# Optimization experiments

Hardware: AMD Instinct MI355X
Metric: run time of the kernel (lower is better)

Reference implementation:

```python
import jax, jax.numpy as jnp
from jax import lax
import numpy as np

NSTART, NOPEN, NHID, NCLOSE, NLAYERS, KSZ, N = 40, 128, 256, 3, 40, 9, 1024
H_STEP = 0.1
PAD = (KSZ - 1) // 2  # 4 -> same-length conv
EPS = 1e-5


def conv1(x, K):
    # x: (1, Cin, N), K: (Cout, Cin, k); cross-correlation like torch F.conv1d
    return lax.conv_general_dilated(x, K, (1,), [(PAD, PAD)],
                                    dimension_numbers=('NCH', 'OIH', 'NCH'))


def conv1T(x, K):
    # torch F.conv_transpose1d(x, K, padding=PAD) == conv1d with swapped-channel,
    # flipped kernel and padding k-1-PAD (= PAD here since k=9, PAD=4)
    Kt = jnp.flip(jnp.swapaxes(K, 0, 1), -1)
    return lax.conv_general_dilated(x, Kt, (1,), [(PAD, PAD)],
                                    dimension_numbers=('NCH', 'OIH', 'NCH'))


def instance_norm(x):
    # x: (1, C, N); normalize per channel over spatial dim, biased var, no affine
    m = jnp.mean(x, axis=-1, keepdims=True)
    v = jnp.var(x, axis=-1, keepdims=True)
    return (x - m) * lax.rsqrt(v + EPS)


def get_graph_lap(Z):
    # Z: (C, N). Normalized Gaussian-affinity graph Laplacian.
    sq = jnp.sum(Z * Z, axis=0)  # (N,)
    D2 = jnp.maximum(sq[:, None] + sq[None, :] - 2.0 * (Z.T @ Z), 0.0)
    sigma = jnp.mean(D2) + 1e-12
    Wg = jnp.exp(-D2 / sigma)
    deg = jnp.sum(Wg, axis=1)
    Dh = lax.rsqrt(deg)
    L = Dh[:, None] * (jnp.diag(deg) - Wg) * Dh[None, :]
    return L, deg


def double_sym_layer(Z, Wi, Bi, L):
    # Z: (nopen, N), Wi: (2, nhid, nopen, 9), Bi: (2, nopen, 1), L: (N, N)
    A0 = instance_norm(conv1((Z + Bi[0])[None], Wi[0]))
    A1 = instance_norm((conv1((Z + Bi[1])[None], Wi[1])[0] @ L)[None])
    A0 = jax.nn.relu(A0)
    A1 = jax.nn.relu(A1)
    A0 = conv1T(A0, Wi[0])[0]
    A1 = conv1T(A1, Wi[1])[0] @ L.T
    return A0 + A1  # (nopen, N)


def setup_inputs() -> dict:
    key = jax.random.key(0)
    k1, k2, k3, k4, k5 = jax.random.split(key, 5)
    Z = jax.random.normal(k1, (NSTART, N), dtype=jnp.float32)
    stdv_o = 0.001 * NOPEN / NSTART
    Kopen = jax.random.uniform(k2, (NOPEN, NSTART), minval=-stdv_o, maxval=stdv_o, dtype=jnp.float32)
    stdv_c = 0.001 * NCLOSE / NOPEN
    Kclose = jax.random.uniform(k3, (NCLOSE, NOPEN), minval=-stdv_c, maxval=stdv_c, dtype=jnp.float32)
    W = jax.random.uniform(k4, (NLAYERS, 2, NHID, NOPEN, KSZ), minval=-1e-4, maxval=1e-4, dtype=jnp.float32)
    Bias = jax.random.uniform(k5, (NLAYERS, 2, NOPEN, 1), dtype=jnp.float32) * 1e-4
    return {"Z": Z, "Kopen": Kopen, "Kclose": Kclose, "W": W, "Bias": Bias}


def reference(Z, Kopen, Kclose, W, Bias):
    h = H_STEP
    Zc = Kopen @ Z          # (nopen, N)
    Zold = Zc
    L, _ = get_graph_lap(Zc)
    for i in range(NLAYERS):
        if i % 10 == 0:
            L, _ = get_graph_lap(Zc)
        Ai = double_sym_layer(Zc, W[i], Bias[i], L)
        Zc, Zold = 2.0 * Zc - Zold - (h * h) * Ai, Zc  # leapfrog step
    return (Kclose @ Zc, Kclose @ Zold)
```

## Files before the change

kernel.cpp:

```cpp
#include <hip/hip_runtime.h>

#define NN 1024
#define NOPEN 128
#define NHID 256
#define NSTART 40
#define NCLOSE 3
#define NLAYERS 40
#define KSZ 9

static constexpr float H2 = 0.01f;
static constexpr float IN_EPS = 1e-5f;

using floatx4 = __attribute__((ext_vector_type(4))) float;
using bfrag = __attribute__((ext_vector_type(8))) short;

__device__ __forceinline__ ushort f2bf(float f) {
    union { float f; unsigned u; } v; v.f = f;
    unsigned r = v.u + 0x7fffu + ((v.u >> 16) & 1u);
    return (ushort)(r >> 16);
}

__device__ __forceinline__ void prepw_piece(const float* __restrict__ W, ushort* __restrict__ Wt,
                                            ushort* __restrict__ WtT, int lb, int lsrc, int tid) {
    if (lb < 72) {
        int q = lb; int coq = q & 3; q >>= 2; int t = q % 9, z = q / 9;
        const float* Wz = W + (size_t)(lsrc * 2 + z) * (NHID * NOPEN * KSZ);
        ushort* Wo = Wt + ((size_t)z * 9 + t) * (NHID * NOPEN);
#pragma unroll
        for (int r = 0; r < 32; ++r) {
            int idx = r * 256 + tid;
            int co = coq * 64 + (idx >> 7), ci = idx & 127;
            Wo[co * NOPEN + ci] = f2bf(Wz[co * (NOPEN * KSZ) + ci * KSZ + t]);
        }
    } else {
        int q = lb - 72; int ciq = q & 3; q >>= 2; int t = q % 9, z = q / 9;
        const float* Wz = W + (size_t)(lsrc * 2 + z) * (NHID * NOPEN * KSZ);
        ushort* Wo = WtT + ((size_t)z * 9 + t) * (NOPEN * NHID);
#pragma unroll
        for (int r = 0; r < 32; ++r) {
            int idx = r * 256 + tid;
            int ci = ciq * 32 + (idx >> 8), co = idx & 255;
            Wo[ci * NHID + co] = f2bf(Wz[co * (NOPEN * KSZ) + ci * KSZ + t]);
        }
    }
}

__global__ __launch_bounds__(256) void k_open(const float* __restrict__ Kopen, const float* __restrict__ Z,
                       float* __restrict__ Zc, float* __restrict__ Zold,
                       const float* __restrict__ Bias0, ushort* __restrict__ Zct,
                       ushort* __restrict__ At0, ushort* __restrict__ At1,
                       const float* __restrict__ W, ushort* __restrict__ Wt,
                       ushort* __restrict__ WtT, float* __restrict__ sig) {
    const int v = blockIdx.x, tid = threadIdx.x;
    if (v < 512) {
        int o = v >> 2, n = (v & 3) * 256 + tid;
        float acc = 0.f;
#pragma unroll
        for (int s = 0; s < NSTART; ++s)
            acc = fmaf(Kopen[o * NSTART + s], Z[s * NN + n], acc);
        Zc[o * NN + n] = acc;
        Zold[o * NN + n] = acc;
#pragma unroll
        for (int z = 0; z < 2; ++z)
            Zct[z * (1032 * 128) + (n + 4) * 128 + o] = f2bf(acc + Bias0[z * NOPEN + o]);
    } else if (v < 656) {
        prepw_piece(W, Wt, WtT, v - 512, 0, tid);
    } else {
        if (tid == 0) sig[0] = 0.f;
        for (int idx = tid; idx < 1024; idx += 256) {
            int z = idx >> 9, rr = idx & 511;
            ushort* Zz = Zct + z * (1032 * 128);
            Zz[rr] = 0; Zz[1028 * 128 + rr] = 0;
        }
        for (int idx = tid; idx < 2048; idx += 256) {
            int a = idx >> 10, rr = idx & 1023;
            ushort* A = a ? At1 : At0;
            A[rr] = 0; A[1028 * 256 + rr] = 0;
        }
    }
}

__global__ __launch_bounds__(256) void k_d2(const float* __restrict__ Zc,
                                            float* __restrict__ D2, float* __restrict__ sig) {
    __shared__ __align__(16) float Zi[32 * 36];
    __shared__ __align__(16) float Zj[32 * 68];
    __shared__ float sqi[32], sqj[64];
    __shared__ float red[4];
    const int tid = threadIdx.x;
    const int tx = tid & 15, ty = tid >> 4;
    const int j0 = blockIdx.x * 64, i0 = blockIdx.y * 32;
    if (tid < 32) sqi[tid] = 0.f;
    else if (tid < 96) sqj[tid - 32] = 0.f;
    float acc[2][4] = {};
    for (int c0 = 0; c0 < NOPEN; c0 += 32) {
        for (int idx = tid; idx < 32 * 32; idx += 256) {
            int c = idx >> 5, ii = idx & 31;
            Zi[c * 36 + ii] = Zc[(c0 + c) * NN + i0 + ii];
        }
        for (int idx = tid; idx < 32 * 64; idx += 256) {
            int c = idx >> 6, jj = idx & 63;
            Zj[c * 68 + jj] = Zc[(c0 + c) * NN + j0 + jj];
        }
        __syncthreads();
        if (tid < 32) {
            float s = 0.f;
            for (int c = 0; c < 32; ++c) { float x = Zi[c * 36 + tid]; s = fmaf(x, x, s); }
            sqi[tid] += s;
        } else if (tid < 96) {
            int jj = tid - 32;
            float s = 0.f;
            for (int c = 0; c < 32; ++c) { float x = Zj[c * 68 + jj]; s = fmaf(x, x, s); }
            sqj[jj] += s;
        }
#pragma unroll 8
        for (int c = 0; c < 32; ++c) {
            float2 zi = *(const float2*)&Zi[c * 36 + ty * 2];
            float4 zj = *(const float4*)&Zj[c * 68 + tx * 4];
            acc[0][0] = fmaf(zi.x, zj.x, acc[0][0]);
            acc[0][1] = fmaf(zi.x, zj.y, acc[0][1]);
            acc[0][2] = fmaf(zi.x, zj.z, acc[0][2]);
            acc[0][3] = fmaf(zi.x, zj.w, acc[0][3]);
            acc[1][0] = fmaf(zi.y, zj.x, acc[1][0]);
            acc[1][1] = fmaf(zi.y, zj.y, acc[1][1]);
            acc[1][2] = fmaf(zi.y, zj.z, acc[1][2]);
            acc[1][3] = fmaf(zi.y, zj.w, acc[1][3]);
        }
        __syncthreads();
    }
    float part = 0.f;
#pragma unroll
    for (int m = 0; m < 2; ++m) {
        int i = i0 + ty * 2 + m;
        float sqi_v = sqi[ty * 2 + m];
        float4 d;
        d.x = fmaxf(sqi_v + sqj[tx * 4 + 0] - 2.f * acc[m][0], 0.f);
        d.y = fmaxf(sqi_v + sqj[tx * 4 + 1] - 2.f * acc[m][1], 0.f);
        d.z = fmaxf(sqi_v + sqj[tx * 4 + 2] - 2.f * acc[m][2], 0.f);
        d.w = fmaxf(sqi_v + sqj[tx * 4 + 3] - 2.f * acc[m][3], 0.f);
        *(float4*)&D2[(size_t)i * NN + j0 + tx * 4] = d;
        part += (d.x + d.y) + (d.z + d.w);
    }
#pragma unroll
    for (int off = 32; off > 0; off >>= 1) part += __shfl_down(part, off);
    if ((tid & 63) == 0) red[tid >> 6] = part;
    __syncthreads();
    if (tid == 0) atomicAdd(sig, red[0] + red[1] + red[2] + red[3]);
}

__global__ void k_deg(const float* __restrict__ D2, const float* __restrict__ sig,
                      float* __restrict__ Dh) {
    __shared__ float red[4];
    int i = blockIdx.x, tid = threadIdx.x;
    float inv = 1.f / (sig[0] * (1.f / 1048576.f) + 1e-12f);
    float4 v = *(const float4*)&D2[(size_t)i * NN + tid * 4];
    float s = __expf(-v.x * inv) + __expf(-v.y * inv) + __expf(-v.z * inv) + __expf(-v.w * inv);
#pragma unroll
    for (int off = 32; off > 0; off >>= 1) s += __shfl_down(s, off);
    if ((tid & 63) == 0) red[tid >> 6] = s;
    __syncthreads();
    if (tid == 0) Dh[i] = rsqrtf(red[0] + red[1] + red[2] + red[3]);
}

__global__ void k_L(const float* __restrict__ D2, const float* __restrict__ sig,
                    const float* __restrict__ Dh, ushort* __restrict__ Lb) {
    int i = blockIdx.x, tid = threadIdx.x;
    int j = tid * 4;
    float inv = 1.f / (sig[0] * (1.f / 1048576.f) + 1e-12f);
    float dhi = Dh[i];
    float4 v = *(const float4*)&D2[(size_t)i * NN + j];
    float4 dj = *(const float4*)&Dh[j];
    float4 o;
    o.x = -dhi * dj.x * __expf(-v.x * inv);
    o.y = -dhi * dj.y * __expf(-v.y * inv);
    o.z = -dhi * dj.z * __expf(-v.z * inv);
    o.w = -dhi * dj.w * __expf(-v.w * inv);
    if (i == j + 0) o.x += 1.f;
    if (i == j + 1) o.y += 1.f;
    if (i == j + 2) o.z += 1.f;
    if (i == j + 3) o.w += 1.f;
    ushort4 ob; ob.x = f2bf(o.x); ob.y = f2bf(o.y); ob.z = f2bf(o.z); ob.w = f2bf(o.w);
    *(ushort4*)&Lb[(size_t)i * NN + j] = ob;
}

__global__ __launch_bounds__(256) void k_conv(const ushort* __restrict__ Zct,
        const ushort* __restrict__ Wt, float* __restrict__ C0, ushort* __restrict__ C1b) {
    const int z = blockIdx.z;
    const int p0 = blockIdx.x * 64, co0 = blockIdx.y * 32;
    __shared__ ushort Xs[72 * 136];
    __shared__ ushort Wl[9 * 32 * 136];
    const int tid = threadIdx.x;
    const ushort* Zz = Zct + z * (1032 * 128);
    const ushort* Wz = Wt + (size_t)z * 9 * NHID * NOPEN;
    for (int idx = tid; idx < 1152; idx += 256) {
        int row = idx >> 4, ch = (idx & 15) * 8;
        *(bfrag*)&Xs[row * 136 + ch] = *(const bfrag*)&Zz[(p0 + row) * 128 + ch];
    }
    for (int idx = tid; idx < 4608; idx += 256) {
        int t = idx >> 9, rem = idx & 511;
        int c = rem >> 4, ch = (rem & 15) * 8;
        *(bfrag*)&Wl[(t * 32 + c) * 136 + ch] = *(const bfrag*)&Wz[(t * NHID + co0 + c) * 128 + ch];
    }
    __syncthreads();
    const int l = tid & 63, wv = tid >> 6;
    const int wm = wv >> 1, wn = wv & 1;
    const int lm = l & 15, lq = l >> 4;
    floatx4 acc[2] = {};
    for (int t = 0; t < 9; ++t) {
        const int wbase = (t * 32 + wm * 16 + lm) * 136 + lq * 8;
        const int xbase = (wn * 32 + lm + t) * 136 + lq * 8;
#pragma unroll
        for (int kc = 0; kc < 4; ++kc) {
            bfrag a = *(const bfrag*)&Wl[wbase + kc * 32];
            bfrag b0 = *(const bfrag*)&Xs[xbase + kc * 32];
            acc[0] = __builtin_amdgcn_mfma_f32_16x16x32_bf16(a, b0, acc[0], 0, 0, 0);
            bfrag b1 = *(const bfrag*)&Xs[xbase + 16 * 136 + kc * 32];
            acc[1] = __builtin_amdgcn_mfma_f32_16x16x32_bf16(a, b1, acc[1], 0, 0, 0);
        }
    }
    const int cog = co0 + wm * 16 + lq * 4;
    const int pg = p0 + wn * 32 + lm;
#pragma unroll
    for (int j = 0; j < 2; ++j)
#pragma unroll
        for (int r = 0; r < 4; ++r) {
            if (z == 0) C0[(cog + r) * NN + pg + j * 16] = acc[j][r];
            else        C1b[(cog + r) * NN + pg + j * 16] = f2bf(acc[j][r]);
        }
}

__global__ __launch_bounds__(256) void k_xl_mfma(const ushort* __restrict__ X,
                                                 const ushort* __restrict__ Lb,
                                                 float* __restrict__ P, int M) {
    __shared__ __align__(16) ushort As[64 * 136];
    __shared__ __align__(16) ushort Bs[128 * 136];
    const int tid = threadIdx.x;
    const int lane = tid & 63, wave = tid >> 6;
    const int wm = wave >> 1, wn = wave & 1;
    const int n0 = blockIdx.x * 128, m0 = blockIdx.y * 64, kc = blockIdx.z * 128;
    {
        int q = tid;
#pragma unroll
        for (int r = 0; r < 4; ++r, q += 256) {
            int row = q >> 4, ch = (q & 15) * 8;
            *(bfrag*)&As[row * 136 + ch] = *(const bfrag*)&X[(m0 + row) * NN + kc + ch];
        }
        q = tid;
#pragma unroll
        for (int r = 0; r < 8; ++r, q += 256) {
            int row = q >> 4, ch = (q & 15) * 8;
            *(bfrag*)&Bs[row * 136 + ch] = *(const bfrag*)&Lb[(n0 + row) * NN + kc + ch];
        }
    }
    __syncthreads();
    floatx4 acc[2][4] = {};
    const int lrow = (lane & 15) * 136;
    const int koff = (lane >> 4) * 8;
#pragma unroll
    for (int ks = 0; ks < 4; ++ks) {
        bfrag a[2], b[4];
#pragma unroll
        for (int i = 0; i < 2; ++i)
            a[i] = *(const bfrag*)&As[(wm * 32 + i * 16) * 136 + lrow + ks * 32 + koff];
#pragma unroll
        for (int j = 0; j < 4; ++j)
            b[j] = *(const bfrag*)&Bs[(wn * 64 + j * 16) * 136 + lrow + ks * 32 + koff];
#pragma unroll
        for (int i = 0; i < 2; ++i)
#pragma unroll
            for (int j = 0; j < 4; ++j)
                acc[i][j] = __builtin_amdgcn_mfma_f32_16x16x32_bf16(a[i], b[j], acc[i][j], 0, 0, 0);
    }
    const int mg0 = m0 + wm * 32 + (lane >> 4) * 4;
    const int ng0 = n0 + wn * 64 + (lane & 15);
    const size_t base = (size_t)blockIdx.z * M * NN;
#pragma unroll
    for (int i = 0; i < 2; ++i)
#pragma unroll
        for (int j = 0; j < 4; ++j)
#pragma unroll
            for (int r = 0; r < 4; ++r)
                P[base + (size_t)(mg0 + i * 16 + r) * NN + ng0 + j * 16] = acc[i][j][r];
}

__global__ void k_inorm(const float* __restrict__ C0, const float* __restrict__ P1,
                        float* __restrict__ A1sum, float* __restrict__ Mu, float* __restrict__ Rs) {
    const int c = blockIdx.x, arr = blockIdx.y, tid = threadIdx.x;
    __shared__ float rs[4], rq[4];
    float4 v;
    if (arr == 0) {
        v = *(const float4*)&C0[c * NN + tid * 4];
    } else {
        v.x = v.y = v.z = v.w = 0.f;
#pragma unroll
        for (int s = 0; s < 8; ++s) {
            float4 p = *(const float4*)&P1[(size_t)(s * NHID + c) * NN + tid * 4];
            v.x += p.x; v.y += p.y; v.z += p.z; v.w += p.w;
        }
        *(float4*)&A1sum[c * NN + tid * 4] = v;
    }
    float s = (v.x + v.y) + (v.z + v.w);
    float q = (v.x * v.x + v.y * v.y) + (v.z * v.z + v.w * v.w);
#pragma unroll
    for (int off = 32; off > 0; off >>= 1) { s += __shfl_down(s, off); q += __shfl_down(q, off); }
    if ((tid & 63) == 0) { rs[tid >> 6] = s; rq[tid >> 6] = q; }
    __syncthreads();
    if (tid == 0) {
        float S = rs[0] + rs[1] + rs[2] + rs[3];
        float Q = rq[0] + rq[1] + rq[2] + rq[3];
        float mean = S * (1.f / NN);
        float var = Q * (1.f / NN) - mean * mean;
        Mu[arr * NHID + c] = mean;
        Rs[arr * NHID + c] = rsqrtf(var + IN_EPS);
    }
}

__global__ __launch_bounds__(256) void k_normT(const float* __restrict__ C0,
        const float* __restrict__ A1sum, const float* __restrict__ Mu, const float* __restrict__ Rs,
        ushort* __restrict__ At0, ushort* __restrict__ At1) {
    const int arr = blockIdx.z;
    const int p0 = blockIdx.x * 64, co0 = blockIdx.y * 64;
    const float* in = arr ? A1sum : C0;
    ushort* out = arr ? At1 : At0;
    __shared__ ushort Ls[64 * 72];
    const int tid = threadIdx.x;
#pragma unroll
    for (int r = 0; r < 4; ++r) {
        int idx = r * 256 + tid;
        int col = idx >> 4, pq = idx & 15;
        int co = co0 + col;
        float4 v = *(const float4*)&in[(size_t)co * NN + p0 + pq * 4];
        float m = Mu[arr * NHID + co], sc = Rs[arr * NHID + co];
        Ls[(pq * 4 + 0) * 72 + col] = f2bf(fmaxf((v.x - m) * sc, 0.f));
        Ls[(pq * 4 + 1) * 72 + col] = f2bf(fmaxf((v.y - m) * sc, 0.f));
        Ls[(pq * 4 + 2) * 72 + col] = f2bf(fmaxf((v.z - m) * sc, 0.f));
        Ls[(pq * 4 + 3) * 72 + col] = f2bf(fmaxf((v.w - m) * sc, 0.f));
    }
    __syncthreads();
#pragma unroll
    for (int r = 0; r < 2; ++r) {
        int idx = r * 256 + tid;
        int row = idx >> 3, ch = (idx & 7) * 8;
        *(bfrag*)&out[(size_t)(p0 + row + 4) * 256 + co0 + ch] = *(const bfrag*)&Ls[row * 72 + ch];
    }
}

__global__ __launch_bounds__(256) void k_convT(const ushort* __restrict__ At0,
        const ushort* __restrict__ At1, const ushort* __restrict__ WtT,
        float* __restrict__ Tacc, ushort* __restrict__ T1b) {
    const int z = blockIdx.z;
    const int p0 = blockIdx.x * 64, ci0 = blockIdx.y * 16;
    __shared__ ushort Al[72 * 264];
    __shared__ ushort Wl[9 * 16 * 264];
    const ushort* A = z ? At1 : At0;
    const ushort* Wz = WtT + (size_t)z * 9 * NOPEN * NHID;
    const int tid = threadIdx.x;
    for (int idx = tid; idx < 2304; idx += 256) {
        int row = idx >> 5, ch = (idx & 31) * 8;
        *(bfrag*)&Al[row * 264 + ch] = *(const bfrag*)&A[(p0 + row) * 256 + ch];
    }
    for (int idx = tid; idx < 4608; idx += 256) {
        int t = idx >> 9, rem = idx & 511;
        int c = rem >> 5, ch = (rem & 31) * 8;
        *(bfrag*)&Wl[(t * 16 + c) * 264 + ch] = *(const bfrag*)&Wz[(t * NOPEN + ci0 + c) * 256 + ch];
    }
    __syncthreads();
    const int l = tid & 63, wv = tid >> 6;
    const int lm = l & 15, lq = l >> 4;
    floatx4 acc0 = {}, acc1 = {};
    for (int t = 0; t < 9; ++t) {
        const int abase = (wv * 16 + lm + 8 - t) * 264 + lq * 8;
        const int wbase = (t * 16 + lm) * 264 + lq * 8;
#pragma unroll
        for (int kc = 0; kc < 8; kc += 2) {
            bfrag a0 = *(const bfrag*)&Wl[wbase + kc * 32];
            bfrag b0 = *(const bfrag*)&Al[abase + kc * 32];
            acc0 = __builtin_amdgcn_mfma_f32_16x16x32_bf16(a0, b0, acc0, 0, 0, 0);
            bfrag a1 = *(const bfrag*)&Wl[wbase + kc * 32 + 32];
            bfrag b1 = *(const bfrag*)&Al[abase + kc * 32 + 32];
            acc1 = __builtin_amdgcn_mfma_f32_16x16x32_bf16(a1, b1, acc1, 0, 0, 0);
        }
    }
    floatx4 acc = acc0 + acc1;
    const int cig = ci0 + lq * 4;
    const int pg = p0 + wv * 16 + lm;
#pragma unroll
    for (int r = 0; r < 4; ++r) {
        if (z == 0) Tacc[(cig + r) * NN + pg] = acc[r];
        else        T1b[(cig + r) * NN + pg] = f2bf(acc[r]);
    }
}

__global__ __launch_bounds__(256) void k_leap(const float* __restrict__ P2,
        const float* __restrict__ Tacc, const float* __restrict__ Zc, float* __restrict__ Zo,
        const float* __restrict__ BiasN, ushort* __restrict__ Zct,
        const float* __restrict__ W, ushort* __restrict__ Wt, ushort* __restrict__ WtT,
        float* __restrict__ sig, int lnext, int doprep) {
    const int v = blockIdx.x, tid = threadIdx.x;
    if (v < 128) {
        int off = (v * 256 + tid) * 4;
        float4 a = *(const float4*)&Tacc[off];
#pragma unroll
        for (int s = 0; s < 8; ++s) {
            float4 p = *(const float4*)&P2[(size_t)(s << 17) + off];
            a.x += p.x; a.y += p.y; a.z += p.z; a.w += p.w;
        }
        float4 zc = *(const float4*)&Zc[off];
        float4 zo = *(const float4*)&Zo[off];
        float4 zn;
        zn.x = 2.f * zc.x - zo.x - H2 * a.x;
        zn.y = 2.f * zc.y - zo.y - H2 * a.y;
        zn.z = 2.f * zc.z - zo.z - H2 * a.z;
        zn.w = 2.f * zc.w - zo.w - H2 * a.w;
        *(float4*)&Zo[off] = zn;
        int ci = off >> 10, n = off & 1023;
#pragma unroll
        for (int z = 0; z < 2; ++z) {
            float bz = BiasN[z * NOPEN + ci];
            ushort* Zz = Zct + z * (1032 * 128);
            Zz[(n + 4) * 128 + ci] = f2bf(zn.x + bz);
            Zz[(n + 5) * 128 + ci] = f2bf(zn.y + bz);
            Zz[(n + 6) * 128 + ci] = f2bf(zn.z + bz);
            Zz[(n + 7) * 128 + ci] = f2bf(zn.w + bz);
        }
    } else if (v < 272) {
        if (doprep) prepw_piece(W, Wt, WtT, v - 128, lnext, tid);
    } else {
        if (tid == 0) sig[0] = 0.f;
    }
}

__global__ void k_close(const float* __restrict__ Kclose, const float* __restrict__ Zc,
                        const float* __restrict__ Zold, float* __restrict__ out) {
    int n = blockIdx.x * 256 + threadIdx.x;
    int o = blockIdx.y;
    const float* Zb = blockIdx.z ? Zold : Zc;
    float a = 0.f;
#pragma unroll
    for (int c = 0; c < NOPEN; ++c) a = fmaf(Kclose[o * NOPEN + c], Zb[c * NN + n], a);
    out[blockIdx.z * (NCLOSE * NN) + o * NN + n] = a;
}

extern "C" void kernel_launch(void* const* d_in, const int* in_sizes, int n_in,
                              void* d_out, int out_size, void* d_ws, size_t ws_size,
                              hipStream_t stream) {
    const float* Z      = (const float*)d_in[0];
    const float* Kopen  = (const float*)d_in[1];
    const float* Kclose = (const float*)d_in[2];
    const float* W      = (const float*)d_in[3];
    const float* Bias   = (const float*)d_in[4];
    float* out = (float*)d_out;
    float* ws  = (float*)d_ws;

    float* Zb0   = ws + 0;
    float* Zb1   = ws + 131072;
    float* D2    = ws + 262144;
    float* C0    = ws + 1310720;
    float* A1sum = ws + 1572864;
    float* Tacc  = ws + 1835008;
    float* P1    = ws + 1966080;
    float* P2    = ws + 4063232;
    float* Dh    = ws + 5111808;
    float* sig   = ws + 5112832;
    float* Mu    = ws + 5113856;
    float* Rs    = ws + 5114880;
    ushort* Lb  = (ushort*)(ws + 5115904);
    ushort* C1b = (ushort*)(ws + 5640192);
    ushort* T1b = (ushort*)(ws + 5771264);
    ushort* Zct = (ushort*)(ws + 5836800);
    ushort* At0 = (ushort*)(ws + 5968896);
    ushort* At1 = (ushort*)(ws + 6100992);
    ushort* Wt  = (ushort*)(ws + 6233088);
    ushort* WtT = (ushort*)(ws + 6528000);

    k_open<<<dim3(657), 256, 0, stream>>>(Kopen, Z, Zb0, Zb1, Bias, Zct, At0, At1,
                                          W, Wt, WtT, sig);

    float* Zc = Zb0;
    float* Zold = Zb1;
    for (int i = 0; i < NLAYERS; ++i) {
        if (i % 10 == 0) {
            k_d2<<<dim3(16, 32), 256, 0, stream>>>(Zc, D2, sig);
            k_deg<<<dim3(NN), 256, 0, stream>>>(D2, sig, Dh);
            k_L<<<dim3(NN), 256, 0, stream>>>(D2, sig, Dh, Lb);
        }
        k_conv<<<dim3(16, 8, 2), 256, 0, stream>>>(Zct, Wt, C0, C1b);
        k_xl_mfma<<<dim3(8, 4, 8), 256, 0, stream>>>(C1b, Lb, P1, NHID);
        k_inorm<<<dim3(NHID, 2), 256, 0, stream>>>(C0, P1, A1sum, Mu, Rs);
        k_normT<<<dim3(16, 4, 2), 256, 0, stream>>>(C0, A1sum, Mu, Rs, At0, At1);
        k_convT<<<dim3(16, 8, 2), 256, 0, stream>>>(At0, At1, WtT, Tacc, T1b);
        k_xl_mfma<<<dim3(8, 2, 8), 256, 0, stream>>>(T1b, Lb, P2, NOPEN);
        int lnext = (i + 1 < NLAYERS) ? i + 1 : NLAYERS - 1;
        k_leap<<<dim3(273), 256, 0, stream>>>(P2, Tacc, Zc, Zold,
                                              Bias + (size_t)lnext * 2 * NOPEN, Zct,
                                              W, Wt, WtT, sig, lnext, (i + 1 < NLAYERS) ? 1 : 0);
        float* tmp = Zc; Zc = Zold; Zold = tmp;
    }

    k_close<<<dim3(4, NCLOSE, 2), 256, 0, stream>>>(Kclose, Zc, Zold, out);
}
```

Baseline: 2.122 ms.

## Restructure layer pipeline: fuse leapfrog into conv, merge norm into GEMM kernels, atomic accumulate

Reworks each layer's kernel sequence. The leapfrog update moves into the next layer's conv input staging, using a 3-buffer rotation and a point-major (n,128) layout for Z. Instance-norm and transpose work is merged into the L-GEMM and convT kernels, and the second L-GEMM accumulates into Tacc with atomics instead of writing split-K partials. This cuts the launches per layer from 7 to 5 and removes the P2, A1sum and Zct buffers. In exchange it adds atomic contention, recomputes the leapfrog expression redundantly in every conv block, and changes summation order.

```diff
diff --git a/kernel.cpp b/kernel.cpp
--- a/kernel.cpp
+++ b/kernel.cpp
@@ -46,11 +46,9 @@
 }
 
 __global__ __launch_bounds__(256) void k_open(const float* __restrict__ Kopen, const float* __restrict__ Z,
-                       float* __restrict__ Zc, float* __restrict__ Zold,
-                       const float* __restrict__ Bias0, ushort* __restrict__ Zct,
-                       ushort* __restrict__ At0, ushort* __restrict__ At1,
+                       float* __restrict__ B0, ushort* __restrict__ At0, ushort* __restrict__ At1,
                        const float* __restrict__ W, ushort* __restrict__ Wt,
-                       ushort* __restrict__ WtT, float* __restrict__ sig) {
+                       ushort* __restrict__ WtT, float* __restrict__ Tacc, float* __restrict__ sig) {
     const int v = blockIdx.x, tid = threadIdx.x;
     if (v < 512) {
         int o = v >> 2, n = (v & 3) * 256 + tid;
@@ -58,29 +56,23 @@
 #pragma unroll
         for (int s = 0; s < NSTART; ++s)
             acc = fmaf(Kopen[o * NSTART + s], Z[s * NN + n], acc);
-        Zc[o * NN + n] = acc;
-        Zold[o * NN + n] = acc;
-#pragma unroll
-        for (int z = 0; z < 2; ++z)
-            Zct[z * (1032 * 128) + (n + 4) * 128 + o] = f2bf(acc + Bias0[z * NOPEN + o]);
+        B0[n * 128 + o] = acc;
     } else if (v < 656) {
         prepw_piece(W, Wt, WtT, v - 512, 0, tid);
-    } else {
+    } else if (v == 656) {
         if (tid == 0) sig[0] = 0.f;
-        for (int idx = tid; idx < 1024; idx += 256) {
-            int z = idx >> 9, rr = idx & 511;
-            ushort* Zz = Zct + z * (1032 * 128);
-            Zz[rr] = 0; Zz[1028 * 128 + rr] = 0;
-        }
         for (int idx = tid; idx < 2048; idx += 256) {
             int a = idx >> 10, rr = idx & 1023;
             ushort* A = a ? At1 : At0;
             A[rr] = 0; A[1028 * 256 + rr] = 0;
         }
-    }
-}
-
-__global__ __launch_bounds__(256) void k_d2(const float* __restrict__ Zc,
+    } else {
+        int w = v - 657;
+        *(float4*)&Tacc[(w * 256 + tid) * 4] = float4{0.f, 0.f, 0.f, 0.f};
+    }
+}
+
+__global__ __launch_bounds__(256) void k_d2(const float* __restrict__ Zcur,
                                             float* __restrict__ D2, float* __restrict__ sig) {
     __shared__ __align__(16) float Zi[32 * 36];
     __shared__ __align__(16) float Zj[32 * 68];
@@ -94,12 +86,12 @@
     float acc[2][4] = {};
     for (int c0 = 0; c0 < NOPEN; c0 += 32) {
         for (int idx = tid; idx < 32 * 32; idx += 256) {
-            int c = idx >> 5, ii = idx & 31;
-            Zi[c * 36 + ii] = Zc[(c0 + c) * NN + i0 + ii];
+            int c = idx & 31, ii = idx >> 5;
+            Zi[c * 36 + ii] = Zcur[(i0 + ii) * 128 + c0 + c];
         }
         for (int idx = tid; idx < 32 * 64; idx += 256) {
-            int c = idx >> 6, jj = idx & 63;
-            Zj[c * 68 + jj] = Zc[(c0 + c) * NN + j0 + jj];
+            int c = idx & 31, jj = idx >> 5;
+            Zj[c * 68 + jj] = Zcur[(j0 + jj) * 128 + c0 + c];
         }
         __syncthreads();
         if (tid < 32) {
@@ -182,23 +174,51 @@
     *(ushort4*)&Lb[(size_t)i * NN + j] = ob;
 }
 
-__global__ __launch_bounds__(256) void k_conv(const ushort* __restrict__ Zct,
+__global__ __launch_bounds__(256) void k_conv2(const float* __restrict__ Zc, const float* __restrict__ Zo,
+        const float* __restrict__ Ta, float* __restrict__ Zn, const float* __restrict__ BiasL,
         const ushort* __restrict__ Wt, float* __restrict__ C0, ushort* __restrict__ C1b) {
     const int z = blockIdx.z;
     const int p0 = blockIdx.x * 64, co0 = blockIdx.y * 32;
     __shared__ ushort Xs[72 * 136];
     __shared__ ushort Wl[9 * 32 * 136];
     const int tid = threadIdx.x;
-    const ushort* Zz = Zct + z * (1032 * 128);
+    const float* Bz = BiasL + z * NOPEN;
     const ushort* Wz = Wt + (size_t)z * 9 * NHID * NOPEN;
-    for (int idx = tid; idx < 1152; idx += 256) {
-        int row = idx >> 4, ch = (idx & 15) * 8;
-        *(bfrag*)&Xs[row * 136 + ch] = *(const bfrag*)&Zz[(p0 + row) * 128 + ch];
+    for (int idx = tid; idx < 72 * 32; idx += 256) {
+        int row = idx >> 5, ci = (idx & 31) * 4;
+        int n = p0 - 4 + row;
+        ushort4 o4 = {0, 0, 0, 0};
+        if ((unsigned)n < (unsigned)NN) {
+            float4 zc = *(const float4*)&Zc[n * 128 + ci];
+            float4 zo = *(const float4*)&Zo[n * 128 + ci];
+            float4 ta = *(const float4*)&Ta[n * 128 + ci];
+            float4 bb = *(const float4*)&Bz[ci];
+            o4.x = f2bf(2.f * zc.x - zo.x - H2 * ta.x + bb.x);
+            o4.y = f2bf(2.f * zc.y - zo.y - H2 * ta.y + bb.y);
+            o4.z = f2bf(2.f * zc.z - zo.z - H2 * ta.z + bb.z);
+            o4.w = f2bf(2.f * zc.w - zo.w - H2 * ta.w + bb.w);
+        }
+        *(ushort4*)&Xs[row * 136 + ci] = o4;
     }
     for (int idx = tid; idx < 4608; idx += 256) {
         int t = idx >> 9, rem = idx & 511;
         int c = rem >> 4, ch = (rem & 15) * 8;
         *(bfrag*)&Wl[(t * 32 + c) * 136 + ch] = *(const bfrag*)&Wz[(t * NHID + co0 + c) * 128 + ch];
+    }
+    if (blockIdx.y == 0 && z == 0) {
+        for (int idx = tid; idx < 64 * 32; idx += 256) {
+            int row = idx >> 5, ci = (idx & 31) * 4;
+            int n = p0 + row;
+            float4 zc = *(const float4*)&Zc[n * 128 + ci];
+            float4 zo = *(const float4*)&Zo[n * 128 + ci];
+            float4 ta = *(const float4*)&Ta[n * 128 + ci];
+            float4 o;
+            o.x = 2.f * zc.x - zo.x - H2 * ta.x;
+            o.y = 2.f * zc.y - zo.y - H2 * ta.y;
+            o.z = 2.f * zc.z - zo.z - H2 * ta.z;
+            o.w = 2.f * zc.w - zo.w - H2 * ta.w;
+            *(float4*)&Zn[n * 128 + ci] = o;
+        }
     }
     __syncthreads();
     const int l = tid & 63, wv = tid >> 6;
@@ -228,21 +248,22 @@
         }
 }
 
-__global__ __launch_bounds__(256) void k_xl_mfma(const ushort* __restrict__ X,
-                                                 const ushort* __restrict__ Lb,
-                                                 float* __restrict__ P, int M) {
-    __shared__ __align__(16) ushort As[64 * 136];
-    __shared__ __align__(16) ushort Bs[128 * 136];
-    const int tid = threadIdx.x;
-    const int lane = tid & 63, wave = tid >> 6;
-    const int wm = wave >> 1, wn = wave & 1;
-    const int n0 = blockIdx.x * 128, m0 = blockIdx.y * 64, kc = blockIdx.z * 128;
-    {
+__global__ __launch_bounds__(256) void k_s2(const ushort* __restrict__ C1b,
+        const ushort* __restrict__ Lb, float* __restrict__ P1,
+        const float* __restrict__ C0, ushort* __restrict__ At0) {
+    __shared__ __align__(16) ushort sm[26112];
+    const int bid = blockIdx.x, tid = threadIdx.x;
+    if (bid < 256) {
+        ushort* As = sm;
+        ushort* Bs = sm + 8704;
+        const int lane = tid & 63, wave = tid >> 6;
+        const int wm = wave >> 1, wn = wave & 1;
+        const int n0 = (bid & 7) * 128, m0 = ((bid >> 3) & 3) * 64, kc = (bid >> 5) * 128;
         int q = tid;
 #pragma unroll
         for (int r = 0; r < 4; ++r, q += 256) {
             int row = q >> 4, ch = (q & 15) * 8;
-            *(bfrag*)&As[row * 136 + ch] = *(const bfrag*)&X[(m0 + row) * NN + kc + ch];
+            *(bfrag*)&As[row * 136 + ch] = *(const bfrag*)&C1b[(m0 + row) * NN + kc + ch];
         }
         q = tid;
 #pragma unroll
@@ -250,110 +271,64 @@
             int row = q >> 4, ch = (q & 15) * 8;
             *(bfrag*)&Bs[row * 136 + ch] = *(const bfrag*)&Lb[(n0 + row) * NN + kc + ch];
         }
-    }
-    __syncthreads();
-    floatx4 acc[2][4] = {};
-    const int lrow = (lane & 15) * 136;
-    const int koff = (lane >> 4) * 8;
-#pragma unroll
-    for (int ks = 0; ks < 4; ++ks) {
-        bfrag a[2], b[4];
+        __syncthreads();
+        floatx4 acc[2][4] = {};
+        const int lrow = (lane & 15) * 136;
+        const int koff = (lane >> 4) * 8;
+#pragma unroll
+        for (int ks = 0; ks < 4; ++ks) {
+            bfrag a[2], b[4];
+#pragma unroll
+            for (int i = 0; i < 2; ++i)
+                a[i] = *(const bfrag*)&As[(wm * 32 + i * 16) * 136 + lrow + ks * 32 + koff];
+#pragma unroll
+            for (int j = 0; j < 4; ++j)
+                b[j] = *(const bfrag*)&Bs[(wn * 64 + j * 16) * 136 + lrow + ks * 32 + koff];
+#pragma unroll
+            for (int i = 0; i < 2; ++i)
+#pragma unroll
+                for (int j = 0; j < 4; ++j)
+                    acc[i][j] = __builtin_amdgcn_mfma_f32_16x16x32_bf16(a[i], b[j], acc[i][j], 0, 0, 0);
+        }
+        const int mg0 = m0 + wm * 32 + (lane >> 4) * 4;
+        const int ng0 = n0 + wn * 64 + (lane & 15);
+        const size_t base = (size_t)(bid >> 5) * NHID * NN;
 #pragma unroll
         for (int i = 0; i < 2; ++i)
-            a[i] = *(const bfrag*)&As[(wm * 32 + i * 16) * 136 + lrow + ks * 32 + koff];
-#pragma unroll
-        for (int j = 0; j < 4; ++j)
-            b[j] = *(const bfrag*)&Bs[(wn * 64 + j * 16) * 136 + lrow + ks * 32 + koff];
-#pragma unroll
-        for (int i = 0; i < 2; ++i)
 #pragma unroll
             for (int j = 0; j < 4; ++j)
-                acc[i][j] = __builtin_amdgcn_mfma_f32_16x16x32_bf16(a[i], b[j], acc[i][j], 0, 0, 0);
-    }
-    const int mg0 = m0 + wm * 32 + (lane >> 4) * 4;
-    const int ng0 = n0 + wn * 64 + (lane & 15);
-    const size_t base = (size_t)blockIdx.z * M * NN;
-#pragma unroll
-    for (int i = 0; i < 2; ++i)
-#pragma unroll
-        for (int j = 0; j < 4; ++j)
-#pragma unroll
-            for (int r = 0; r < 4; ++r)
-                P[base + (size_t)(mg0 + i * 16 + r) * NN + ng0 + j * 16] = acc[i][j][r];
-}
-
-__global__ void k_inorm(const float* __restrict__ C0, const float* __restrict__ P1,
-                        float* __restrict__ A1sum, float* __restrict__ Mu, float* __restrict__ Rs) {
-    const int c = blockIdx.x, arr = blockIdx.y, tid = threadIdx.x;
-    __shared__ float rs[4], rq[4];
-    float4 v;
-    if (arr == 0) {
-        v = *(const float4*)&C0[c * NN + tid * 4];
-    } else {
-        v.x = v.y = v.z = v.w = 0.f;
-#pragma unroll
-        for (int s = 0; s < 8; ++s) {
-            float4 p = *(const float4*)&P1[(size_t)(s * NHID + c) * NN + tid * 4];
-            v.x += p.x; v.y += p.y; v.z += p.z; v.w += p.w;
-        }
-        *(float4*)&A1sum[c * NN + tid * 4] = v;
-    }
-    float s = (v.x + v.y) + (v.z + v.w);
-    float q = (v.x * v.x + v.y * v.y) + (v.z * v.z + v.w * v.w);
-#pragma unroll
-    for (int off = 32; off > 0; off >>= 1) { s += __shfl_down(s, off); q += __shfl_down(q, off); }
-    if ((tid & 63) == 0) { rs[tid >> 6] = s; rq[tid >> 6] = q; }
-    __syncthreads();
-    if (tid == 0) {
+#pragma unroll
+                for (int r = 0; r < 4; ++r)
+                    P1[base + (size_t)(mg0 + i * 16 + r) * NN + ng0 + j * 16] = acc[i][j][r];
+    } else {
+        float* rs = (float*)sm;
+        float* rq = rs + 4;
+        const int c = bid - 256;
+        float4 v = *(const float4*)&C0[(size_t)c * NN + tid * 4];
+        float s = (v.x + v.y) + (v.z + v.w);
+        float qq = (v.x * v.x + v.y * v.y) + (v.z * v.z + v.w * v.w);
+#pragma unroll
+        for (int off = 32; off > 0; off >>= 1) { s += __shfl_down(s, off); qq += __shfl_down(qq, off); }
+        if ((tid & 63) == 0) { rs[tid >> 6] = s; rq[tid >> 6] = qq; }
+        __syncthreads();
         float S = rs[0] + rs[1] + rs[2] + rs[3];
         float Q = rq[0] + rq[1] + rq[2] + rq[3];
         float mean = S * (1.f / NN);
-        float var = Q * (1.f / NN) - mean * mean;
-        Mu[arr * NHID + c] = mean;
-        Rs[arr * NHID + c] = rsqrtf(var + IN_EPS);
-    }
-}
-
-__global__ __launch_bounds__(256) void k_normT(const float* __restrict__ C0,
-        const float* __restrict__ A1sum, const float* __restrict__ Mu, const float* __restrict__ Rs,
-        ushort* __restrict__ At0, ushort* __restrict__ At1) {
-    const int arr = blockIdx.z;
-    const int p0 = blockIdx.x * 64, co0 = blockIdx.y * 64;
-    const float* in = arr ? A1sum : C0;
-    ushort* out = arr ? At1 : At0;
-    __shared__ ushort Ls[64 * 72];
-    const int tid = threadIdx.x;
-#pragma unroll
-    for (int r = 0; r < 4; ++r) {
-        int idx = r * 256 + tid;
-        int col = idx >> 4, pq = idx & 15;
-        int co = co0 + col;
-        float4 v = *(const float4*)&in[(size_t)co * NN + p0 + pq * 4];
-        float m = Mu[arr * NHID + co], sc = Rs[arr * NHID + co];
-        Ls[(pq * 4 + 0) * 72 + col] = f2bf(fmaxf((v.x - m) * sc, 0.f));
-        Ls[(pq * 4 + 1) * 72 + col] = f2bf(fmaxf((v.y - m) * sc, 0.f));
-        Ls[(pq * 4 + 2) * 72 + col] = f2bf(fmaxf((v.z - m) * sc, 0.f));
-        Ls[(pq * 4 + 3) * 72 + col] = f2bf(fmaxf((v.w - m) * sc, 0.f));
-    }
-    __syncthreads();
-#pragma unroll
-    for (int r = 0; r < 2; ++r) {
-        int idx = r * 256 + tid;
-        int row = idx >> 3, ch = (idx & 7) * 8;
-        *(bfrag*)&out[(size_t)(p0 + row + 4) * 256 + co0 + ch] = *(const bfrag*)&Ls[row * 72 + ch];
-    }
-}
-
-__global__ __launch_bounds__(256) void k_convT(const ushort* __restrict__ At0,
-        const ushort* __restrict__ At1, const ushort* __restrict__ WtT,
-        float* __restrict__ Tacc, ushort* __restrict__ T1b) {
-    const int z = blockIdx.z;
-    const int p0 = blockIdx.x * 64, ci0 = blockIdx.y * 16;
-    __shared__ ushort Al[72 * 264];
-    __shared__ ushort Wl[9 * 16 * 264];
-    const ushort* A = z ? At1 : At0;
-    const ushort* Wz = WtT + (size_t)z * 9 * NOPEN * NHID;
-    const int tid = threadIdx.x;
+        float rstd = rsqrtf(Q * (1.f / NN) - mean * mean + IN_EPS);
+        int p = tid * 4;
+        At0[(p + 4) * 256 + c] = f2bf(fmaxf((v.x - mean) * rstd, 0.f));
+        At0[(p + 5) * 256 + c] = f2bf(fmaxf((v.y - mean) * rstd, 0.f));
+        At0[(p + 6) * 256 + c] = f2bf(fmaxf((v.z - mean) * rstd, 0.f));
+        At0[(p + 7) * 256 + c] = f2bf(fmaxf((v.w - mean) * rstd, 0.f));
+    }
+}
+
+__device__ __forceinline__ void convT_body(int b, const ushort* __restrict__ A,
+        const ushort* __restrict__ Wz, ushort* sm, int tid, floatx4& acc, int& cig, int& pg) {
+    const int pt = b & 15, cit = b >> 4;
+    const int p0 = pt * 64, ci0 = cit * 16;
+    ushort* Al = sm;
+    ushort* Wl = sm + 19008;
     for (int idx = tid; idx < 2304; idx += 256) {
         int row = idx >> 5, ch = (idx & 31) * 8;
         *(bfrag*)&Al[row * 264 + ch] = *(const bfrag*)&A[(p0 + row) * 256 + ch];
@@ -380,64 +355,150 @@
             acc1 = __builtin_amdgcn_mfma_f32_16x16x32_bf16(a1, b1, acc1, 0, 0, 0);
         }
     }
-    floatx4 acc = acc0 + acc1;
-    const int cig = ci0 + lq * 4;
-    const int pg = p0 + wv * 16 + lm;
-#pragma unroll
-    for (int r = 0; r < 4; ++r) {
-        if (z == 0) Tacc[(cig + r) * NN + pg] = acc[r];
-        else        T1b[(cig + r) * NN + pg] = f2bf(acc[r]);
-    }
-}
-
-__global__ __launch_bounds__(256) void k_leap(const float* __restrict__ P2,
-        const float* __restrict__ Tacc, const float* __restrict__ Zc, float* __restrict__ Zo,
-        const float* __restrict__ BiasN, ushort* __restrict__ Zct,
-        const float* __restrict__ W, ushort* __restrict__ Wt, ushort* __restrict__ WtT,
-        float* __restrict__ sig, int lnext, int doprep) {
-    const int v = blockIdx.x, tid = threadIdx.x;
-    if (v < 128) {
-        int off = (v * 256 + tid) * 4;
-        float4 a = *(const float4*)&Tacc[off];
+    acc = acc0 + acc1;
+    cig = ci0 + lq * 4;
+    pg = p0 + wv * 16 + lm;
+}
+
+__global__ __launch_bounds__(256) void k_s3(const ushort* __restrict__ At0,
+        const ushort* __restrict__ WtT, float* __restrict__ Tacc,
+        const float* __restrict__ P1, ushort* __restrict__ At1) {
+    __shared__ __align__(16) ushort sm[57024];
+    const int bid = blockIdx.x, tid = threadIdx.x;
+    if (bid < 128) {
+        floatx4 acc; int cig, pg;
+        convT_body(bid, At0, WtT, sm, tid, acc, cig, pg);
+#pragma unroll
+        for (int r = 0; r < 4; ++r)
+            Tacc[pg * 128 + cig + r] = acc[r];
+    } else {
+        float* rs = (float*)sm;
+        float* rq = rs + 4;
+        const int c = bid - 128;
+        float4 v = {0.f, 0.f, 0.f, 0.f};
 #pragma unroll
         for (int s = 0; s < 8; ++s) {
-            float4 p = *(const float4*)&P2[(size_t)(s << 17) + off];
-            a.x += p.x; a.y += p.y; a.z += p.z; a.w += p.w;
-        }
-        float4 zc = *(const float4*)&Zc[off];
-        float4 zo = *(const float4*)&Zo[off];
-        float4 zn;
-        zn.x = 2.f * zc.x - zo.x - H2 * a.x;
-        zn.y = 2.f * zc.y - zo.y - H2 * a.y;
-        zn.z = 2.f * zc.z - zo.z - H2 * a.z;
-        zn.w = 2.f * zc.w - zo.w - H2 * a.w;
-        *(float4*)&Zo[off] = zn;
-        int ci = off >> 10, n = off & 1023;
-#pragma unroll
-        for (int z = 0; z < 2; ++z) {
-            float bz = BiasN[z * NOPEN + ci];
-            ushort* Zz = Zct + z * (1032 * 128);
-            Zz[(n + 4) * 128 + ci] = f2bf(zn.x + bz);
-            Zz[(n + 5) * 128 + ci] = f2bf(zn.y + bz);
-            Zz[(n + 6) * 128 + ci] = f2bf(zn.z + bz);
-            Zz[(n + 7) * 128 + ci] = f2bf(zn.w + bz);
-        }
-    } else if (v < 272) {
-        if (doprep) prepw_piece(W, Wt, WtT, v - 128, lnext, tid);
+            float4 p = *(const float4*)&P1[(size_t)(s * NHID + c) * NN + tid * 4];
+            v.x += p.x; v.y += p.y; v.z += p.z; v.w += p.w;
+        }
+        float s = (v.x + v.y) + (v.z + v.w);
+        float qq = (v.x * v.x + v.y * v.y) + (v.z * v.z + v.w * v.w);
+#pragma unroll
+        for (int off = 32; off > 0; off >>= 1) { s += __shfl_down(s, off); qq += __shfl_down(qq, off); }
+        if ((tid & 63) == 0) { rs[tid >> 6] = s; rq[tid >> 6] = qq; }
+        __syncthreads();
+        float S = rs[0] + rs[1] + rs[2] + rs[3];
+        float Q = rq[0] + rq[1] + rq[2] + rq[3];
+        float mean = S * (1.f / NN);
+        float rstd = rsqrtf(Q * (1.f / NN) - mean * mean + IN_EPS);
+        int p = tid * 4;
+        At1[(p + 4) * 256 + c] = f2bf(fmaxf((v.x - mean) * rstd, 0.f));
+        At1[(p + 5) * 256 + c] = f2bf(fmaxf((v.y - mean) * rstd, 0.f));
+        At1[(p + 6) * 256 + c] = f2bf(fmaxf((v.z - mean) * rstd, 0.f));
+        At1[(p + 7) * 256 + c] = f2bf(fmaxf((v.w - mean) * rstd, 0.f));
+    }
+}
+
+__global__ __launch_bounds__(256) void k_s4(const ushort* __restrict__ At1,
+        const ushort* __restrict__ WtT, ushort* __restrict__ T1b,
+        const float* __restrict__ W, ushort* __restrict__ Wt, ushort* __restrict__ WtT_w,
+        int lnext, int doprep) {
+    __shared__ __align__(16) ushort sm[57024];
+    const int bid = blockIdx.x, tid = threadIdx.x;
+    if (bid < 128) {
+        floatx4 acc; int cig, pg;
+        convT_body(bid, At1, WtT + (size_t)9 * NOPEN * NHID, sm, tid, acc, cig, pg);
+#pragma unroll
+        for (int r = 0; r < 4; ++r)
+            T1b[(cig + r) * NN + pg] = f2bf(acc[r]);
+    } else {
+        if (doprep) prepw_piece(W, Wt, WtT_w, bid - 128, lnext, tid);
+    }
+}
+
+__global__ __launch_bounds__(256) void k_s5(const ushort* __restrict__ T1b,
+        const ushort* __restrict__ Lb, float* __restrict__ Tacc, float* __restrict__ sig) {
+    __shared__ __align__(16) ushort sm[26112];
+    const int bid = blockIdx.x, tid = threadIdx.x;
+    if (bid < 128) {
+        ushort* As = sm;
+        ushort* Bs = sm + 8704;
+        const int lane = tid & 63, wave = tid >> 6;
+        const int wm = wave >> 1, wn = wave & 1;
+        const int n0 = (bid & 7) * 128, m0 = ((bid >> 3) & 1) * 64, kc = (bid >> 4) * 128;
+        int q = tid;
+#pragma unroll
+        for (int r = 0; r < 4; ++r, q += 256) {
+            int row = q >> 4, ch = (q & 15) * 8;
+            *(bfrag*)&As[row * 136 + ch] = *(const bfrag*)&T1b[(m0 + row) * NN + kc + ch];
+        }
+        q = tid;
+#pragma unroll
+        for (int r = 0; r < 8; ++r, q += 256) {
+            int row = q >> 4, ch = (q & 15) * 8;
+            *(bfrag*)&Bs[row * 136 + ch] = *(const bfrag*)&Lb[(n0 + row) * NN + kc + ch];
+        }
+        __syncthreads();
+        floatx4 acc[2][4] = {};
+        const int lrow = (lane & 15) * 136;
+        const int koff = (lane >> 4) * 8;
+#pragma unroll
+        for (int ks = 0; ks < 4; ++ks) {
+            bfrag a[2], b[4];
+#pragma unroll
+            for (int i = 0; i < 2; ++i)
+                a[i] = *(const bfrag*)&As[(wm * 32 + i * 16) * 136 + lrow + ks * 32 + koff];
+#pragma unroll
+            for (int j = 0; j < 4; ++j)
+                b[j] = *(const bfrag*)&Bs[(wn * 64 + j * 16) * 136 + lrow + ks * 32 + koff];
+#pragma unroll
+            for (int i = 0; i < 2; ++i)
+#pragma unroll
+                for (int j = 0; j < 4; ++j)
+                    acc[i][j] = __builtin_amdgcn_mfma_f32_16x16x32_bf16(a[i], b[j], acc[i][j], 0, 0, 0);
+        }
+        const int mg0 = m0 + wm * 32 + (lane >> 4) * 4;
+        const int ng0 = n0 + wn * 64 + (lane & 15);
+#pragma unroll
+        for (int i = 0; i < 2; ++i)
+#pragma unroll
+            for (int j = 0; j < 4; ++j)
+#pragma unroll
+                for (int r = 0; r < 4; ++r)
+                    atomicAdd(&Tacc[(ng0 + j * 16) * 128 + mg0 + i * 16 + r], acc[i][j][r]);
     } else {
         if (tid == 0) sig[0] = 0.f;
     }
 }
 
 __global__ void k_close(const float* __restrict__ Kclose, const float* __restrict__ Zc,
-                        const float* __restrict__ Zold, float* __restrict__ out) {
+                        const float* __restrict__ Zo, const float* __restrict__ Ta,
+                        float* __restrict__ out) {
     int n = blockIdx.x * 256 + threadIdx.x;
-    int o = blockIdx.y;
-    const float* Zb = blockIdx.z ? Zold : Zc;
+    int o = blockIdx.y, zsel = blockIdx.z;
     float a = 0.f;
-#pragma unroll
-    for (int c = 0; c < NOPEN; ++c) a = fmaf(Kclose[o * NOPEN + c], Zb[c * NN + n], a);
-    out[blockIdx.z * (NCLOSE * NN) + o * NN + n] = a;
+    if (zsel == 0) {
+#pragma unroll
+        for (int c4 = 0; c4 < 32; ++c4) {
+            float4 zc = *(const float4*)&Zc[n * 128 + c4 * 4];
+            float4 zo = *(const float4*)&Zo[n * 128 + c4 * 4];
+            float4 ta = *(const float4*)&Ta[n * 128 + c4 * 4];
+            float4 k = *(const float4*)&Kclose[o * 128 + c4 * 4];
+            a = fmaf(k.x, 2.f * zc.x - zo.x - H2 * ta.x, a);
+            a = fmaf(k.y, 2.f * zc.y - zo.y - H2 * ta.y, a);
+            a = fmaf(k.z, 2.f * zc.z - zo.z - H2 * ta.z, a);
+            a = fmaf(k.w, 2.f * zc.w - zo.w - H2 * ta.w, a);
+        }
+    } else {
+#pragma unroll
+        for (int c4 = 0; c4 < 32; ++c4) {
+            float4 zc = *(const float4*)&Zc[n * 128 + c4 * 4];
+            float4 k = *(const float4*)&Kclose[o * 128 + c4 * 4];
+            a = fmaf(k.x, zc.x, a); a = fmaf(k.y, zc.y, a);
+            a = fmaf(k.z, zc.z, a); a = fmaf(k.w, zc.w, a);
+        }
+    }
+    out[zsel * (NCLOSE * NN) + o * NN + n] = a;
 }
 
 extern "C" void kernel_launch(void* const* d_in, const int* in_sizes, int n_in,
@@ -451,50 +512,50 @@
     float* out = (float*)d_out;
     float* ws  = (float*)d_ws;
 
-    float* Zb0   = ws + 0;
-    float* Zb1   = ws + 131072;
-    float* D2    = ws + 262144;
-    float* C0    = ws + 1310720;
-    float* A1sum = ws + 1572864;
-    float* Tacc  = ws + 1835008;
-    float* P1    = ws + 1966080;
-    float* P2    = ws + 4063232;
-    float* Dh    = ws + 5111808;
-    float* sig   = ws + 5112832;
-    float* Mu    = ws + 5113856;
-    float* Rs    = ws + 5114880;
-    ushort* Lb  = (ushort*)(ws + 5115904);
-    ushort* C1b = (ushort*)(ws + 5640192);
-    ushort* T1b = (ushort*)(ws + 5771264);
-    ushort* Zct = (ushort*)(ws + 5836800);
-    ushort* At0 = (ushort*)(ws + 5968896);
-    ushort* At1 = (ushort*)(ws + 6100992);
-    ushort* Wt  = (ushort*)(ws + 6233088);
-    ushort* WtT = (ushort*)(ws + 6528000);
-
-    k_open<<<dim3(657), 256, 0, stream>>>(Kopen, Z, Zb0, Zb1, Bias, Zct, At0, At1,
-                                          W, Wt, WtT, sig);
-
-    float* Zc = Zb0;
-    float* Zold = Zb1;
-    for (int i = 0; i < NLAYERS; ++i) {
-        if (i % 10 == 0) {
-            k_d2<<<dim3(16, 32), 256, 0, stream>>>(Zc, D2, sig);
+    float* B0   = ws + 0;
+    float* B1   = ws + 131072;
+    float* B2   = ws + 262144;
+    float* Tacc = ws + 393216;
+    float* D2   = ws + 524288;
+    float* C0   = ws + 1572864;
+    float* P1   = ws + 1835008;
+    float* Dh   = ws + 3932160;
+    float* sig  = ws + 3933184;
+    ushort* Lb  = (ushort*)(ws + 3934208);
+    ushort* C1b = (ushort*)(ws + 4458496);
+    ushort* T1b = (ushort*)(ws + 4589568);
+    ushort* At0 = (ushort*)(ws + 4655104);
+    ushort* At1 = (ushort*)(ws + 4787200);
+    ushort* Wt  = (ushort*)(ws + 4919296);
+    ushort* WtT = (ushort*)(ws + 5214208);
+
+    k_open<<<dim3(785), 256, 0, stream>>>(Kopen, Z, B0, At0, At1, W, Wt, WtT, Tacc, sig);
+
+    float* bufs[3] = {B0, B1, B2};
+    int ic = 0, io = 0;
+    for (int l = 0; l < NLAYERS; ++l) {
+        int in_ = 3 - ((ic == io) ? (ic + ic) % 3 : (ic + io))
+                  ;
+        if (ic == io) in_ = (ic + 1) % 3;
+        else in_ = 3 - ic - io;
+        float* Zc = bufs[ic];
+        float* Zo = bufs[io];
+        float* Zn = bufs[in_];
+
+        k_conv2<<<dim3(16, 8, 2), 256, 0, stream>>>(Zc, Zo, Tacc, Zn,
+                Bias + (size_t)l * 2 * NOPEN, Wt, C0, C1b);
+        if (l % 10 == 0) {
+            k_d2<<<dim3(16, 32), 256, 0, stream>>>(Zn, D2, sig);
             k_deg<<<dim3(NN), 256, 0, stream>>>(D2, sig, Dh);
             k_L<<<dim3(NN), 256, 0, stream>>>(D2, sig, Dh, Lb);
         }
-        k_conv<<<dim3(16, 8, 2), 256, 0, stream>>>(Zct, Wt, C0, C1b);
-        k_xl_mfma<<<dim3(8, 4, 8), 256, 0, stream>>>(C1b, Lb, P1, NHID);
-        k_inorm<<<dim3(NHID, 2), 256, 0, stream>>>(C0, P1, A1sum, Mu, Rs);
-        k_normT<<<dim3(16, 4, 2), 256, 0, stream>>>(C0, A1sum, Mu, Rs, At0, At1);
-        k_convT<<<dim3(16, 8, 2), 256, 0, stream>>>(At0, At1, WtT, Tacc, T1b);
-        k_xl_mfma<<<dim3(8, 2, 8), 256, 0, stream>>>(T1b, Lb, P2, NOPEN);
-        int lnext = (i + 1 < NLAYERS) ? i + 1 : NLAYERS - 1;
-        k_leap<<<dim3(273), 256, 0, stream>>>(P2, Tacc, Zc, Zold,
-                                              Bias + (size_t)lnext * 2 * NOPEN, Zct,
-                                              W, Wt, WtT, sig, lnext, (i + 1 < NLAYERS) ? 1 : 0);
-        float* tmp = Zc; Zc = Zold; Zold = tmp;
-    }
-
-    k_close<<<dim3(4, NCLOSE, 2), 256, 0, stream>>>(Kclose, Zc, Zold, out);
-}
+        k_s2<<<dim3(512), 256, 0, stream>>>(C1b, Lb, P1, C0, At0);
+        k_s3<<<dim3(384), 256, 0, stream>>>(At0, WtT, Tacc, P1, At1);
+        int lnext = (l + 1 < NLAYERS) ? l + 1 : l;
+        k_s4<<<dim3(272), 256, 0, stream>>>(At1, WtT, T1b, W, Wt, WtT,
+                                            lnext, (l + 1 < NLAYERS) ? 1 : 0);
+        k_s5<<<dim3(129), 256, 0, stream>>>(T1b, Lb, Tacc, sig);
+        io = ic; ic = in_;
+    }
+    k_close<<<dim3(4, NCLOSE, 2), 256, 0, stream>>>(Kclose, bufs[ic], bufs[io], Tacc, out);
+}
```

New measurement: 2.896 ms. +36.4%, slower.
